# Kernel optimization log

Hardware: AMD Instinct MI355X
Metric: run time of the kernel (lower is better)

Reference implementation:

```python
import jax, jax.numpy as jnp
import numpy as np

B, S, D_MODEL = 4, 4096, 1024
H, KD, F = 16, 64, 256
KERNEL_SCALE = 1.0
NORM = 1.0 / np.sqrt(KD).astype(np.float32)  # 1/sqrt(key_dim)
EPS = 1e-6


def setup_inputs() -> dict:
    key = jax.random.key(0)
    ks = jax.random.split(key, 12)
    s = 0.02
    x = jax.random.normal(ks[0], (B, S, D_MODEL), dtype=jnp.float32)
    Wq = jax.random.normal(ks[1], (D_MODEL, H * KD), dtype=jnp.float32) * s
    bq = jnp.zeros((H * KD,), jnp.float32)
    Wk = jax.random.normal(ks[2], (D_MODEL, H * KD), dtype=jnp.float32) * s
    bk = jnp.zeros((H * KD,), jnp.float32)
    Wv = jax.random.normal(ks[3], (D_MODEL, H * KD), dtype=jnp.float32) * s
    bv = jnp.zeros((H * KD,), jnp.float32)
    # RFF params (non-trainable in original; orthogonal-ish random here)
    rff_W = jax.random.normal(ks[4], (KD, F), dtype=jnp.float32)
    q_, _ = jnp.linalg.qr(rff_W.T)  # (F, KD) -> orthonormal rows subset
    rff_W = q_.T[:KD, :F].astype(jnp.float32)
    rff_b = jax.random.uniform(ks[5], (F,), jnp.float32, 0.0, 2.0 * np.pi)
    Wo = jax.random.normal(ks[6], (H * KD, D_MODEL), dtype=jnp.float32) * s
    bo = jnp.zeros((D_MODEL,), jnp.float32)
    return {"x": x, "Wq": Wq, "bq": bq, "Wk": Wk, "bk": bk, "Wv": Wv,
            "bv": bv, "rff_W": rff_W, "rff_b": rff_b, "Wo": Wo, "bo": bo}


def _split_heads(t):
    # [B, S, H*KD] -> [B, H, S, KD]
    return t.reshape(B, S, H, KD).transpose(0, 2, 1, 3)


def _rff(t, rff_W, rff_b):
    # RandomFourierFeatures: cos((x*scale) @ W + b) * sqrt(2/F)
    proj = jnp.einsum('bhsd,df->bhsf', t * KERNEL_SCALE, rff_W) + rff_b
    return jnp.cos(proj) * np.sqrt(2.0 / F).astype(np.float32)


def reference(x, Wq, bq, Wk, bk, Wv, bv, rff_W, rff_b, Wo, bo):
    q = _split_heads(x @ Wq + bq)  # [B,H,S,KD]
    k = _split_heads(x @ Wk + bk)
    v = _split_heads(x @ Wv + bv)
    q_prime = _rff(q * NORM, rff_W, rff_b)  # [B,H,S,F]
    k_prime = _rff(k * NORM, rff_W, rff_b)
    # Non-causal FAVOR+ linear attention: O(L)
    kv = jnp.einsum('bhsf,bhsd->bhfd', k_prime, v)          # [B,H,F,KD]
    k_sum = jnp.sum(k_prime, axis=2)                         # [B,H,F]
    num = jnp.einsum('bhsf,bhfd->bhsd', q_prime, kv)         # [B,H,S,KD]
    den = jnp.einsum('bhsf,bhf->bhs', q_prime, k_sum)        # [B,H,S]
    out = num / (den + EPS)[..., None]
    out = out.transpose(0, 2, 1, 3).reshape(B, S, H * KD)    # merge heads
    return out @ Wo + bo
```

## Files before the change

### kernel.cpp

```cpp
#include <hip/hip_runtime.h>
#include <hip/hip_bf16.h>
#include <math.h>

#define B_SZ    4
#define S_LEN   4096
#define DMODEL  1024
#define NH      16
#define KDIM    64
#define NF      256
#define NROWS   (B_SZ * S_LEN)
#define RFF_SCALE 0.08838834764831845f
#define NORM_Q    0.125f

typedef __attribute__((ext_vector_type(8))) short s8v;
typedef __attribute__((ext_vector_type(4))) float f4v;

static __device__ __forceinline__ unsigned short f2bf(float f) {
  unsigned u = __float_as_uint(f);
  unsigned r = (u + 0x7FFFu + ((u >> 16) & 1u)) >> 16;
  return (unsigned short)r;
}

#define MFMA16(a, b, c) __builtin_amdgcn_mfma_f32_16x16x32_bf16((a), (b), (c), 0, 0, 0)

__device__ __forceinline__ void glds16(const void* g, void* l) {
  __builtin_amdgcn_global_load_lds(
      (const __attribute__((address_space(1))) void*)g,
      (__attribute__((address_space(3))) void*)l, 16, 0, 0);
}

__global__ __launch_bounds__(256) void cast_bf16_kernel(
    const float* __restrict__ src, unsigned short* __restrict__ dst, int n8)
{
  int i = blockIdx.x * 256 + threadIdx.x;
  if (i >= n8) return;
  const float* s = src + (size_t)i * 8;
  float4 a = *(const float4*)s;
  float4 b = *(const float4*)(s + 4);
  union { s8v v; unsigned short u[8]; } o;
  o.u[0]=f2bf(a.x); o.u[1]=f2bf(a.y); o.u[2]=f2bf(a.z); o.u[3]=f2bf(a.w);
  o.u[4]=f2bf(b.x); o.u[5]=f2bf(b.y); o.u[6]=f2bf(b.z); o.u[7]=f2bf(b.w);
  *(s8v*)(dst + (size_t)i * 8) = o.v;
}

__global__ __launch_bounds__(256) void transpose_cast_kernel(
    const float* __restrict__ W, unsigned short* __restrict__ WT)
{
  __shared__ float t[32][33];
  const int k0 = blockIdx.y * 32, n0 = blockIdx.x * 32;
  const int c = threadIdx.x & 31, r4 = threadIdx.x >> 5;
#pragma unroll
  for (int i = 0; i < 4; ++i) {
    int row = r4 + i * 8;
    t[row][c] = W[(size_t)(k0 + row) * 1024 + n0 + c];
  }
  __syncthreads();
#pragma unroll
  for (int i = 0; i < 4; ++i) {
    int row = r4 + i * 8;
    WT[(size_t)(n0 + row) * 1024 + k0 + c] = f2bf(t[c][row]);
  }
}

__global__ __launch_bounds__(256) void prep_rff_kernel(
    const float* __restrict__ rffW, unsigned short* __restrict__ rffWT)
{
  int i = blockIdx.x * 256 + threadIdx.x;
  int f = i >> 6, d = i & 63;
  rffWT[(size_t)f * 64 + d] = f2bf(rffW[(size_t)d * 256 + f] * NORM_Q);
}

template <int OUT_BF16, int QKV_FUSED>
__global__ __launch_bounds__(512, 2) void gemm_bt_kernel(
    const unsigned short* __restrict__ A,
    const unsigned short* __restrict__ BT0,
    const unsigned short* __restrict__ BT1,
    const unsigned short* __restrict__ BT2,
    const float* __restrict__ bias0, const float* __restrict__ bias1,
    const float* __restrict__ bias2,
    void* __restrict__ out0, void* __restrict__ out1, void* __restrict__ out2,
    int M, int N, int K, int NXT)
{
  __shared__ __align__(16) unsigned short As[2][16384];
  __shared__ __align__(16) unsigned short Bs[2][16384];
  const int tid = threadIdx.x;
  const int lane = tid & 63, wave = tid >> 6;

  int wg = blockIdx.x;
  {
    const int nwg = gridDim.x;
    const int q = nwg >> 3, r = nwg & 7;
    const int xcd = wg & 7, pos = wg >> 3;
    wg = (xcd < r ? xcd * (q + 1) : r * (q + 1) + (xcd - r) * q) + pos;
  }
  const int m0 = (wg / NXT) * 256;
  int ngl = (wg % NXT) * 256;
  const unsigned short* BT = BT0;
  const float* bias = bias0;
  void* outp = out0;
  if (QKV_FUSED) {
    int which = ngl >> 10;
    if (which == 1) { BT = BT1; bias = bias1; outp = out1; }
    else if (which == 2) { BT = BT2; bias = bias2; outp = out2; }
    ngl &= 1023;
  }
  const int n0 = ngl;

  const int trow = tid >> 3;
  const int g8 = (((lane & 7) ^ (trow & 7)) * 8);
  const unsigned short* aPtr = A  + (size_t)(m0 + trow) * K + g8;
  const unsigned short* bPtr = BT + (size_t)(n0 + trow) * K + g8;
  const int NT = K >> 6;

  auto STAGE = [&](int ts, int h) {
    if (ts >= NT) return;
    const int buf = ts & 1, half = h >> 1;
    const size_t go = (size_t)half * 128 * K + (size_t)ts * 64;
    if ((h & 1) == 0) {
      unsigned short* lp = &As[buf][half * 8192 + wave * 512];
      glds16(aPtr + go, lp);
      glds16(aPtr + go + (size_t)64 * K, lp + 4096);
    } else {
      unsigned short* lp = &Bs[buf][half * 8192 + wave * 512];
      glds16(bPtr + go, lp);
      glds16(bPtr + go + (size_t)64 * K, lp + 4096);
    }
  };

  const int col = lane & 15, quad = lane >> 4;
  const int wm = (wave >> 2) * 128;
  const int wn = (wave & 3) * 64;
  const int c7 = col & 7;
  const int idxA0 = (wm + col) * 64 + ((quad ^ c7) * 8);
  const int idxA1 = (wm + col) * 64 + (((4 + quad) ^ c7) * 8);
  const int idxB0 = (wn + col) * 64 + ((quad ^ c7) * 8);
  const int idxB1 = (wn + col) * 64 + (((4 + quad) ^ c7) * 8);

  f4v acc[2][4][4];
  const f4v zz = {0.f, 0.f, 0.f, 0.f};
#pragma unroll
  for (int h = 0; h < 2; ++h)
#pragma unroll
    for (int i = 0; i < 4; ++i)
#pragma unroll
      for (int j = 0; j < 4; ++j) acc[h][i][j] = zz;

  STAGE(0, 0); STAGE(0, 1); STAGE(0, 2); STAGE(0, 3);
  asm volatile("s_waitcnt vmcnt(4)" ::: "memory");
  STAGE(1, 0); STAGE(1, 1); STAGE(1, 2);
  asm volatile("s_waitcnt vmcnt(6)" ::: "memory");
  __builtin_amdgcn_s_barrier();

  for (int t = 0; t < NT; ++t) {
    const int buf = t & 1;
    const unsigned short* pA = As[buf];
    const unsigned short* pB = Bs[buf];
    s8v a0[4][2], a1[4][2], b0[2][2], b1[2][2];

#pragma unroll
    for (int x = 0; x < 4; ++x) {
      a0[x][0] = *(const s8v*)&pA[idxA0 + x * 1024];
      a0[x][1] = *(const s8v*)&pA[idxA1 + x * 1024];
    }
#pragma unroll
    for (int u = 0; u < 2; ++u) {
      b0[u][0] = *(const s8v*)&pB[idxB0 + u * 1024];
      b0[u][1] = *(const s8v*)&pB[idxB1 + u * 1024];
    }
    STAGE(t + 1, 3);
    __builtin_amdgcn_s_barrier();
    asm volatile("s_waitcnt lgkmcnt(0)" ::: "memory");
    __builtin_amdgcn_sched_barrier(0);
    __builtin_amdgcn_s_setprio(1);
#pragma unroll
    for (int x = 0; x < 4; ++x)
#pragma unroll
      for (int u = 0; u < 2; ++u) {
        acc[0][x][u] = MFMA16(a0[x][0], b0[u][0], acc[0][x][u]);
        acc[0][x][u] = MFMA16(a0[x][1], b0[u][1], acc[0][x][u]);
      }
    __builtin_amdgcn_s_setprio(0);
    __builtin_amdgcn_sched_barrier(0);
    __builtin_amdgcn_s_barrier();

#pragma unroll
    for (int x = 0; x < 4; ++x) {
      a1[x][0] = *(const s8v*)&pA[idxA0 + 4096 + x * 1024];
      a1[x][1] = *(const s8v*)&pA[idxA1 + 4096 + x * 1024];
    }
    STAGE(t + 2, 0);
    __builtin_amdgcn_s_barrier();
    asm volatile("s_waitcnt lgkmcnt(0)" ::: "memory");
    __builtin_amdgcn_sched_barrier(0);
    __builtin_amdgcn_s_setprio(1);
#pragma unroll
    for (int x = 0; x < 4; ++x)
#pragma unroll
      for (int u = 0; u < 2; ++u) {
        acc[1][x][u] = MFMA16(a1[x][0], b0[u][0], acc[1][x][u]);
        acc[1][x][u] = MFMA16(a1[x][1], b0[u][1], acc[1][x][u]);
      }
    __builtin_amdgcn_s_setprio(0);
    __builtin_amdgcn_sched_barrier(0);
    __builtin_amdgcn_s_barrier();

#pragma unroll
    for (int u = 0; u < 2; ++u) {
      b1[u][0] = *(const s8v*)&pB[idxB0 + 2048 + u * 1024];
      b1[u][1] = *(const s8v*)&pB[idxB1 + 2048 + u * 1024];
    }
    STAGE(t + 2, 1);
    __builtin_amdgcn_s_barrier();
    asm volatile("s_waitcnt lgkmcnt(0)" ::: "memory");
    __builtin_amdgcn_sched_barrier(0);
    __builtin_amdgcn_s_setprio(1);
#pragma unroll
    for (int x = 0; x < 4; ++x)
#pragma unroll
      for (int u = 0; u < 2; ++u) {
        acc[1][x][2 + u] = MFMA16(a1[x][0], b1[u][0], acc[1][x][2 + u]);
        acc[1][x][2 + u] = MFMA16(a1[x][1], b1[u][1], acc[1][x][2 + u]);
      }
    __builtin_amdgcn_s_setprio(0);
    __builtin_amdgcn_sched_barrier(0);
    __builtin_amdgcn_s_barrier();

    STAGE(t + 2, 2);
    __builtin_amdgcn_s_barrier();
    asm volatile("s_waitcnt lgkmcnt(0)" ::: "memory");
    __builtin_amdgcn_sched_barrier(0);
    __builtin_amdgcn_s_setprio(1);
#pragma unroll
    for (int x = 0; x < 4; ++x)
#pragma unroll
      for (int u = 0; u < 2; ++u) {
        acc[0][x][2 + u] = MFMA16(a0[x][0], b1[u][0], acc[0][x][2 + u]);
        acc[0][x][2 + u] = MFMA16(a0[x][1], b1[u][1], acc[0][x][2 + u]);
      }
    __builtin_amdgcn_s_setprio(0);
    __builtin_amdgcn_sched_barrier(0);
    if (t < NT - 2) asm volatile("s_waitcnt vmcnt(6)" ::: "memory");
    else            asm volatile("s_waitcnt vmcnt(0)" ::: "memory");
    __builtin_amdgcn_s_barrier();
  }

#pragma unroll
  for (int h = 0; h < 2; ++h) {
#pragma unroll
    for (int i = 0; i < 4; ++i) {
#pragma unroll
      for (int j = 0; j < 4; ++j) {
        int n = n0 + wn + j * 16 + col;
        float bv = bias[n];
#pragma unroll
        for (int r = 0; r < 4; ++r) {
          int m = m0 + wm + h * 64 + i * 16 + quad * 4 + r;
          float v = acc[h][i][j][r] + bv;
          if (OUT_BF16)
            ((unsigned short*)outp)[(size_t)m * N + n] = f2bf(v);
          else
            ((float*)outp)[(size_t)m * N + n] = v;
        }
      }
    }
  }
}

__global__ __launch_bounds__(256) void kv_kernel(
    const unsigned short* __restrict__ kg, const unsigned short* __restrict__ vg,
    const unsigned short* __restrict__ rffWT, const float* __restrict__ rffb,
    float* __restrict__ pkv)
{
  __shared__ __align__(16) unsigned short vT[80 * 72];
  __shared__ __align__(16) unsigned short kps[256 * 72];
  const int bh = blockIdx.x, chunk = blockIdx.y;
  const int b = bh >> 4, h = bh & 15;
  const int tid = threadIdx.x;
  const int lane = tid & 63, wave = tid >> 6;
  const int col = lane & 15, quad = lane >> 4;
  const f4v zz = {0.f, 0.f, 0.f, 0.f};

  s8v wf[2][4];
  float bfv[4];
#pragma unroll
  for (int ks = 0; ks < 2; ++ks)
#pragma unroll
    for (int t = 0; t < 4; ++t)
      wf[ks][t] = *(const s8v*)(rffWT +
          (size_t)(wave * 64 + t * 16 + col) * 64 + ks * 32 + quad * 8);
#pragma unroll
  for (int j = 0; j < 4; ++j) bfv[j] = rffb[wave * 64 + j * 16 + col];

  for (int e = tid; e < 1024; e += 256) {
    int r = 64 + (e >> 6), s = e & 63;
    vT[r * 72 + s] = (r == 64) ? (unsigned short)0x3F80 : (unsigned short)0;
  }

  f4v kvacc[4][5];
#pragma unroll
  for (int i = 0; i < 4; ++i)
#pragma unroll
    for (int j = 0; j < 5; ++j) kvacc[i][j] = zz;

  for (int st = 0; st < 4; ++st) {
    const int s0 = chunk * 256 + st * 64;
    __syncthreads();
#pragma unroll
    for (int i = 0; i < 2; ++i) {
      int c = tid + i * 256;
      int s = c & 63, ch = c >> 6;
      union { s8v v; unsigned short u[8]; } vv;
      vv.v = *(const s8v*)(vg + ((size_t)(b * S_LEN + s0 + s)) * DMODEL + h * KDIM + ch * 8);
#pragma unroll
      for (int j = 0; j < 8; ++j) vT[(ch * 8 + j) * 72 + s] = vv.u[j];
    }
    f4v p[4][4];
#pragma unroll
    for (int i = 0; i < 4; ++i)
#pragma unroll
      for (int j = 0; j < 4; ++j) p[i][j] = zz;
#pragma unroll
    for (int ks = 0; ks < 2; ++ks) {
      s8v af[4];
#pragma unroll
      for (int t = 0; t < 4; ++t)
        af[t] = *(const s8v*)(kg +
            ((size_t)(b * S_LEN + s0 + t * 16 + col)) * DMODEL + h * KDIM + ks * 32 + quad * 8);
#pragma unroll
      for (int i = 0; i < 4; ++i)
#pragma unroll
        for (int j = 0; j < 4; ++j) p[i][j] = MFMA16(af[i], wf[ks][j], p[i][j]);
    }
#pragma unroll
    for (int j = 0; j < 4; ++j) {
      int f = wave * 64 + j * 16 + col;
#pragma unroll
      for (int i = 0; i < 4; ++i)
#pragma unroll
        for (int r = 0; r < 4; ++r) {
          int s = i * 16 + quad * 4 + r;
          kps[f * 72 + s] = f2bf(__cosf(p[i][j][r] + bfv[j]) * RFF_SCALE);
        }
    }
    __syncthreads();
#pragma unroll
    for (int ks = 0; ks < 2; ++ks) {
      s8v af[4], bf[5];
#pragma unroll
      for (int t = 0; t < 4; ++t)
        af[t] = *(const s8v*)&kps[(wave * 64 + t * 16 + col) * 72 + ks * 32 + quad * 8];
#pragma unroll
      for (int t = 0; t < 5; ++t)
        bf[t] = *(const s8v*)&vT[(t * 16 + col) * 72 + ks * 32 + quad * 8];
#pragma unroll
      for (int i = 0; i < 4; ++i)
#pragma unroll
        for (int j = 0; j < 5; ++j)
          kvacc[i][j] = MFMA16(af[i], bf[j], kvacc[i][j]);
    }
  }
  const size_t base = ((size_t)(chunk * 64 + bh)) * NF * 80;
#pragma unroll
  for (int i = 0; i < 4; ++i)
#pragma unroll
    for (int r = 0; r < 4; ++r) {
      int f = wave * 64 + i * 16 + quad * 4 + r;
#pragma unroll
      for (int j = 0; j < 5; ++j)
        pkv[base + (size_t)f * 80 + j * 16 + col] = kvacc[i][j][r];
    }
}

__global__ __launch_bounds__(256) void reduce_kv_kernel(
    const float* __restrict__ pkv, unsigned short* __restrict__ kvT)
{
  __shared__ unsigned short lt[80 * 256];
  const int bh = blockIdx.x;
  for (int e = threadIdx.x; e < NF * 80; e += 256) {
    float s = 0.f;
#pragma unroll
    for (int c = 0; c < 16; ++c)
      s += pkv[((size_t)(c * 64 + bh)) * NF * 80 + e];
    int f = e / 80, d = e - f * 80;
    lt[d * 256 + f] = f2bf(s);
  }
  __syncthreads();
  for (int o = threadIdx.x; o < 80 * NF; o += 256)
    kvT[(size_t)bh * 80 * NF + o] = lt[o];
}

__global__ __launch_bounds__(256) void attn_kernel(
    const unsigned short* __restrict__ qg, const unsigned short* __restrict__ kvTg,
    const unsigned short* __restrict__ rffWT, const float* __restrict__ rffb,
    unsigned short* __restrict__ att)
{
  __shared__ __align__(16) unsigned short qps[64 * 264];
  __shared__ __align__(16) unsigned short kvs[80 * 264];
  const int bh = blockIdx.x;
  const int b = bh >> 4, h = bh & 15;
  const int tid = threadIdx.x;
  const int lane = tid & 63, wave = tid >> 6;
  const int col = lane & 15, quad = lane >> 4;
  const f4v zz = {0.f, 0.f, 0.f, 0.f};

  s8v wf[2][4];
  float bfv[4];
#pragma unroll
  for (int ks = 0; ks < 2; ++ks)
#pragma unroll
    for (int t = 0; t < 4; ++t)
      wf[ks][t] = *(const s8v*)(rffWT +
          (size_t)(wave * 64 + t * 16 + col) * 64 + ks * 32 + quad * 8);
#pragma unroll
  for (int j = 0; j < 4; ++j) bfv[j] = rffb[wave * 64 + j * 16 + col];

  for (int c = tid; c < 2560; c += 256) {
    int d = c >> 5, ch = c & 31;
    *(s8v*)&kvs[d * 264 + ch * 8] =
        *(const s8v*)(kvTg + (size_t)bh * 80 * NF + d * 256 + ch * 8);
  }

  for (int it = 0; it < 4; ++it) {
    const int s0 = (blockIdx.y * 4 + it) * 64;
    f4v p[4][4];
#pragma unroll
    for (int i = 0; i < 4; ++i)
#pragma unroll
      for (int j = 0; j < 4; ++j) p[i][j] = zz;
#pragma unroll
    for (int ks = 0; ks < 2; ++ks) {
      s8v af[4];
#pragma unroll
      for (int t = 0; t < 4; ++t)
        af[t] = *(const s8v*)(qg +
            ((size_t)(b * S_LEN + s0 + t * 16 + col)) * DMODEL + h * KDIM + ks * 32 + quad * 8);
#pragma unroll
      for (int i = 0; i < 4; ++i)
#pragma unroll
        for (int j = 0; j < 4; ++j) p[i][j] = MFMA16(af[i], wf[ks][j], p[i][j]);
    }
    __syncthreads();
#pragma unroll
    for (int j = 0; j < 4; ++j) {
      int f = wave * 64 + j * 16 + col;
#pragma unroll
      for (int i = 0; i < 4; ++i)
#pragma unroll
        for (int r = 0; r < 4; ++r) {
          int s = i * 16 + quad * 4 + r;
          qps[s * 264 + f] = f2bf(__cosf(p[i][j][r] + bfv[j]) * RFF_SCALE);
        }
    }
    __syncthreads();
    f4v acc[5];
#pragma unroll
    for (int j = 0; j < 5; ++j) acc[j] = zz;
#pragma unroll
    for (int k0 = 0; k0 < 256; k0 += 32) {
      s8v af = *(const s8v*)&qps[(wave * 16 + col) * 264 + k0 + quad * 8];
      s8v bf[5];
#pragma unroll
      for (int t = 0; t < 5; ++t)
        bf[t] = *(const s8v*)&kvs[(t * 16 + col) * 264 + k0 + quad * 8];
#pragma unroll
      for (int j = 0; j < 5; ++j) acc[j] = MFMA16(af, bf[j], acc[j]);
    }
    float inv[4];
#pragma unroll
    for (int r = 0; r < 4; ++r) {
      float den = __shfl(acc[4][r], lane & 48);
      inv[r] = 1.0f / (den + 1e-6f);
    }
#pragma unroll
    for (int r = 0; r < 4; ++r) {
      int m = s0 + wave * 16 + quad * 4 + r;
      size_t obase = ((size_t)(b * S_LEN + m)) * DMODEL + h * KDIM;
#pragma unroll
      for (int j = 0; j < 4; ++j)
        att[obase + j * 16 + col] = f2bf(acc[j][r] * inv[r]);
    }
  }
}

extern "C" void kernel_launch(void* const* d_in, const int* in_sizes, int n_in,
                              void* d_out, int out_size, void* d_ws, size_t ws_size,
                              hipStream_t stream)
{
  const float* x    = (const float*)d_in[0];
  const float* Wq   = (const float*)d_in[1];
  const float* bq   = (const float*)d_in[2];
  const float* Wk   = (const float*)d_in[3];
  const float* bk   = (const float*)d_in[4];
  const float* Wv   = (const float*)d_in[5];
  const float* bv   = (const float*)d_in[6];
  const float* rffW = (const float*)d_in[7];
  const float* rffb = (const float*)d_in[8];
  const float* Wo   = (const float*)d_in[9];
  const float* bo   = (const float*)d_in[10];
  float* out = (float*)d_out;

  char* w = (char*)d_ws;
  const size_t XB = (size_t)NROWS * DMODEL * 2;
  const size_t WT = (size_t)DMODEL * DMODEL * 2;
  unsigned short* xb   = (unsigned short*)(w);
  unsigned short* WqT  = (unsigned short*)(w + XB);
  unsigned short* WkT  = (unsigned short*)(w + XB + WT);
  unsigned short* WvT  = (unsigned short*)(w + XB + 2 * WT);
  unsigned short* WoT  = (unsigned short*)(w + XB + 3 * WT);
  unsigned short* rWT  = (unsigned short*)(w + XB + 4 * WT);
  char* p = w + XB + 4 * WT + 65536;
  unsigned short* qb = (unsigned short*)(p);
  unsigned short* kb = (unsigned short*)(p + XB);
  unsigned short* vb = (unsigned short*)(p + 2 * XB);
  float* pkv         = (float*)(p + 3 * XB);
  unsigned short* kvT = (unsigned short*)(p + 3 * XB + (size_t)16 * 64 * NF * 80 * 4);
  unsigned short* att = kb;

  cast_bf16_kernel<<<NROWS * DMODEL / 8 / 256, 256, 0, stream>>>(x, xb, NROWS * DMODEL / 8);
  dim3 tg(32, 32);
  transpose_cast_kernel<<<tg, 256, 0, stream>>>(Wq, WqT);
  transpose_cast_kernel<<<tg, 256, 0, stream>>>(Wk, WkT);
  transpose_cast_kernel<<<tg, 256, 0, stream>>>(Wv, WvT);
  transpose_cast_kernel<<<tg, 256, 0, stream>>>(Wo, WoT);
  prep_rff_kernel<<<64, 256, 0, stream>>>(rffW, rWT);

  gemm_bt_kernel<1, 1><<<768, 512, 0, stream>>>(
      xb, WqT, WkT, WvT, bq, bk, bv, qb, kb, vb, NROWS, DMODEL, DMODEL, 12);

  kv_kernel<<<dim3(64, 16), 256, 0, stream>>>(kb, vb, rWT, rffb, pkv);
  reduce_kv_kernel<<<64, 256, 0, stream>>>(pkv, kvT);
  attn_kernel<<<dim3(64, 16), 256, 0, stream>>>(qb, kvT, rWT, rffb, att);

  gemm_bt_kernel<0, 0><<<256, 512, 0, stream>>>(
      att, WoT, nullptr, nullptr, bo, nullptr, nullptr, out, nullptr, nullptr,
      NROWS, DMODEL, DMODEL, 4);
}
```

Baseline: 428.9 us.

## Software-pipeline GEMM LDS reads, prefetch K/V/Q tiles, halve chunk counts

The GEMM main loop is reordered so the next tile's A/B fragments are read from LDS at the end of each iteration, and the MFMA phases are regrouped with fewer barriers. The kv and attn kernels now prefetch the next 64-row K/V/Q tile into registers while the current one is computed. They also process 512 rows per block instead of 256, so each launch has half as many blocks. The reduce kernel is split across four blocks per head and sums 8 partial chunks instead of 16, and k' stores are packed into 64-bit writes. The extra prefetch registers may lower occupancy, and fewer blocks reduce parallelism in the attention kernels.

```diff
diff --git a/kernel.cpp b/kernel.cpp
--- a/kernel.cpp
+++ b/kernel.cpp
@@ -9,6 +9,7 @@
 #define KDIM    64
 #define NF      256
 #define NROWS   (B_SZ * S_LEN)
+#define NCHUNK  8
 #define RFF_SCALE 0.08838834764831845f
 #define NORM_Q    0.125f
 
@@ -146,30 +147,47 @@
       for (int j = 0; j < 4; ++j) acc[h][i][j] = zz;
 
   STAGE(0, 0); STAGE(0, 1); STAGE(0, 2); STAGE(0, 3);
-  asm volatile("s_waitcnt vmcnt(4)" ::: "memory");
   STAGE(1, 0); STAGE(1, 1); STAGE(1, 2);
   asm volatile("s_waitcnt vmcnt(6)" ::: "memory");
   __builtin_amdgcn_s_barrier();
+
+  s8v a0[4][2], a1[4][2], b0[2][2], b1[2][2];
+  {
+    const unsigned short* pA = As[0];
+    const unsigned short* pB = Bs[0];
+#pragma unroll
+    for (int u = 0; u < 2; ++u) {
+      b0[u][0] = *(const s8v*)&pB[idxB0 + u * 1024];
+      b0[u][1] = *(const s8v*)&pB[idxB1 + u * 1024];
+    }
+#pragma unroll
+    for (int x = 0; x < 4; ++x) {
+      a0[x][0] = *(const s8v*)&pA[idxA0 + x * 1024];
+      a0[x][1] = *(const s8v*)&pA[idxA1 + x * 1024];
+    }
+  }
 
   for (int t = 0; t < NT; ++t) {
     const int buf = t & 1;
     const unsigned short* pA = As[buf];
     const unsigned short* pB = Bs[buf];
-    s8v a0[4][2], a1[4][2], b0[2][2], b1[2][2];
-
-#pragma unroll
-    for (int x = 0; x < 4; ++x) {
-      a0[x][0] = *(const s8v*)&pA[idxA0 + x * 1024];
-      a0[x][1] = *(const s8v*)&pA[idxA1 + x * 1024];
-    }
-#pragma unroll
-    for (int u = 0; u < 2; ++u) {
-      b0[u][0] = *(const s8v*)&pB[idxB0 + u * 1024];
-      b0[u][1] = *(const s8v*)&pB[idxB1 + u * 1024];
-    }
-    STAGE(t + 1, 3);
+    const unsigned short* qA = As[buf ^ 1];
+    const unsigned short* qB = Bs[buf ^ 1];
+
     __builtin_amdgcn_s_barrier();
     asm volatile("s_waitcnt lgkmcnt(0)" ::: "memory");
+    __builtin_amdgcn_sched_barrier(0);
+#pragma unroll
+    for (int u = 0; u < 2; ++u) {
+      b1[u][0] = *(const s8v*)&pB[idxB0 + 2048 + u * 1024];
+      b1[u][1] = *(const s8v*)&pB[idxB1 + 2048 + u * 1024];
+    }
+    __builtin_amdgcn_sched_barrier(0);
+#pragma unroll
+    for (int x = 0; x < 4; ++x) {
+      a1[x][0] = *(const s8v*)&pA[idxA0 + 4096 + x * 1024];
+      a1[x][1] = *(const s8v*)&pA[idxA1 + 4096 + x * 1024];
+    }
     __builtin_amdgcn_sched_barrier(0);
     __builtin_amdgcn_s_setprio(1);
 #pragma unroll
@@ -181,16 +199,55 @@
       }
     __builtin_amdgcn_s_setprio(0);
     __builtin_amdgcn_sched_barrier(0);
+
     __builtin_amdgcn_s_barrier();
-
+    STAGE(t + 1, 3);
+    asm volatile("s_waitcnt lgkmcnt(8)" ::: "memory");
+    __builtin_amdgcn_sched_barrier(0);
+    __builtin_amdgcn_s_setprio(1);
+#pragma unroll
+    for (int x = 0; x < 4; ++x)
+#pragma unroll
+      for (int u = 0; u < 2; ++u) {
+        acc[0][x][2 + u] = MFMA16(a0[x][0], b1[u][0], acc[0][x][2 + u]);
+        acc[0][x][2 + u] = MFMA16(a0[x][1], b1[u][1], acc[0][x][2 + u]);
+      }
+    __builtin_amdgcn_s_setprio(0);
+    __builtin_amdgcn_sched_barrier(0);
+
+    __builtin_amdgcn_s_barrier();
+    STAGE(t + 2, 1);
+    asm volatile("s_waitcnt lgkmcnt(0)" ::: "memory");
+    __builtin_amdgcn_sched_barrier(0);
+    __builtin_amdgcn_s_setprio(1);
+#pragma unroll
+    for (int x = 0; x < 4; ++x)
+#pragma unroll
+      for (int u = 0; u < 2; ++u) {
+        acc[1][x][2 + u] = MFMA16(a1[x][0], b1[u][0], acc[1][x][2 + u]);
+        acc[1][x][2 + u] = MFMA16(a1[x][1], b1[u][1], acc[1][x][2 + u]);
+      }
+    __builtin_amdgcn_s_setprio(0);
+    __builtin_amdgcn_sched_barrier(0);
+
+    __builtin_amdgcn_s_barrier();
+    STAGE(t + 2, 0);
+    STAGE(t + 2, 2);
+    if (t < NT - 2) asm volatile("s_waitcnt vmcnt(6)" ::: "memory");
+    else            asm volatile("s_waitcnt vmcnt(0)" ::: "memory");
+    __builtin_amdgcn_sched_barrier(0);
+    s8v b0n[2][2], a0n[4][2];
+#pragma unroll
+    for (int u = 0; u < 2; ++u) {
+      b0n[u][0] = *(const s8v*)&qB[idxB0 + u * 1024];
+      b0n[u][1] = *(const s8v*)&qB[idxB1 + u * 1024];
+    }
+    __builtin_amdgcn_sched_barrier(0);
 #pragma unroll
     for (int x = 0; x < 4; ++x) {
-      a1[x][0] = *(const s8v*)&pA[idxA0 + 4096 + x * 1024];
-      a1[x][1] = *(const s8v*)&pA[idxA1 + 4096 + x * 1024];
-    }
-    STAGE(t + 2, 0);
-    __builtin_amdgcn_s_barrier();
-    asm volatile("s_waitcnt lgkmcnt(0)" ::: "memory");
+      a0n[x][0] = *(const s8v*)&qA[idxA0 + x * 1024];
+      a0n[x][1] = *(const s8v*)&qA[idxA1 + x * 1024];
+    }
     __builtin_amdgcn_sched_barrier(0);
     __builtin_amdgcn_s_setprio(1);
 #pragma unroll
@@ -202,46 +259,10 @@
       }
     __builtin_amdgcn_s_setprio(0);
     __builtin_amdgcn_sched_barrier(0);
-    __builtin_amdgcn_s_barrier();
-
-#pragma unroll
-    for (int u = 0; u < 2; ++u) {
-      b1[u][0] = *(const s8v*)&pB[idxB0 + 2048 + u * 1024];
-      b1[u][1] = *(const s8v*)&pB[idxB1 + 2048 + u * 1024];
-    }
-    STAGE(t + 2, 1);
-    __builtin_amdgcn_s_barrier();
-    asm volatile("s_waitcnt lgkmcnt(0)" ::: "memory");
-    __builtin_amdgcn_sched_barrier(0);
-    __builtin_amdgcn_s_setprio(1);
-#pragma unroll
-    for (int x = 0; x < 4; ++x)
-#pragma unroll
-      for (int u = 0; u < 2; ++u) {
-        acc[1][x][2 + u] = MFMA16(a1[x][0], b1[u][0], acc[1][x][2 + u]);
-        acc[1][x][2 + u] = MFMA16(a1[x][1], b1[u][1], acc[1][x][2 + u]);
-      }
-    __builtin_amdgcn_s_setprio(0);
-    __builtin_amdgcn_sched_barrier(0);
-    __builtin_amdgcn_s_barrier();
-
-    STAGE(t + 2, 2);
-    __builtin_amdgcn_s_barrier();
-    asm volatile("s_waitcnt lgkmcnt(0)" ::: "memory");
-    __builtin_amdgcn_sched_barrier(0);
-    __builtin_amdgcn_s_setprio(1);
-#pragma unroll
-    for (int x = 0; x < 4; ++x)
-#pragma unroll
-      for (int u = 0; u < 2; ++u) {
-        acc[0][x][2 + u] = MFMA16(a0[x][0], b1[u][0], acc[0][x][2 + u]);
-        acc[0][x][2 + u] = MFMA16(a0[x][1], b1[u][1], acc[0][x][2 + u]);
-      }
-    __builtin_amdgcn_s_setprio(0);
-    __builtin_amdgcn_sched_barrier(0);
-    if (t < NT - 2) asm volatile("s_waitcnt vmcnt(6)" ::: "memory");
-    else            asm volatile("s_waitcnt vmcnt(0)" ::: "memory");
-    __builtin_amdgcn_s_barrier();
+#pragma unroll
+    for (int u = 0; u < 2; ++u) { b0[u][0] = b0n[u][0]; b0[u][1] = b0n[u][1]; }
+#pragma unroll
+    for (int x = 0; x < 4; ++x) { a0[x][0] = a0n[x][0]; a0[x][1] = a0n[x][1]; }
   }
 
 #pragma unroll
@@ -302,45 +323,66 @@
 #pragma unroll
     for (int j = 0; j < 5; ++j) kvacc[i][j] = zz;
 
-  for (int st = 0; st < 4; ++st) {
-    const int s0 = chunk * 256 + st * 64;
+  const int sA = tid & 63,        chA = tid >> 6;
+  const int sB = (tid + 256) & 63, chB = (tid + 256) >> 6;
+
+  union U { s8v v; unsigned short u[8]; };
+  U v0, v1;
+  s8v kf[2][4];
+  {
+    const int s0 = chunk * 512;
+    v0.v = *(const s8v*)(vg + ((size_t)(b * S_LEN + s0 + sA)) * DMODEL + h * KDIM + chA * 8);
+    v1.v = *(const s8v*)(vg + ((size_t)(b * S_LEN + s0 + sB)) * DMODEL + h * KDIM + chB * 8);
+#pragma unroll
+    for (int ks = 0; ks < 2; ++ks)
+#pragma unroll
+      for (int t = 0; t < 4; ++t)
+        kf[ks][t] = *(const s8v*)(kg +
+            ((size_t)(b * S_LEN + s0 + t * 16 + col)) * DMODEL + h * KDIM + ks * 32 + quad * 8);
+  }
+
+  for (int st = 0; st < 8; ++st) {
+    const int s0 = chunk * 512 + st * 64;
     __syncthreads();
 #pragma unroll
-    for (int i = 0; i < 2; ++i) {
-      int c = tid + i * 256;
-      int s = c & 63, ch = c >> 6;
-      union { s8v v; unsigned short u[8]; } vv;
-      vv.v = *(const s8v*)(vg + ((size_t)(b * S_LEN + s0 + s)) * DMODEL + h * KDIM + ch * 8);
-#pragma unroll
-      for (int j = 0; j < 8; ++j) vT[(ch * 8 + j) * 72 + s] = vv.u[j];
-    }
+    for (int j = 0; j < 8; ++j) vT[(chA * 8 + j) * 72 + sA] = v0.u[j];
+#pragma unroll
+    for (int j = 0; j < 8; ++j) vT[(chB * 8 + j) * 72 + sB] = v1.u[j];
     f4v p[4][4];
 #pragma unroll
     for (int i = 0; i < 4; ++i)
 #pragma unroll
       for (int j = 0; j < 4; ++j) p[i][j] = zz;
 #pragma unroll
-    for (int ks = 0; ks < 2; ++ks) {
-      s8v af[4];
-#pragma unroll
-      for (int t = 0; t < 4; ++t)
-        af[t] = *(const s8v*)(kg +
-            ((size_t)(b * S_LEN + s0 + t * 16 + col)) * DMODEL + h * KDIM + ks * 32 + quad * 8);
+    for (int ks = 0; ks < 2; ++ks)
 #pragma unroll
       for (int i = 0; i < 4; ++i)
 #pragma unroll
-        for (int j = 0; j < 4; ++j) p[i][j] = MFMA16(af[i], wf[ks][j], p[i][j]);
+        for (int j = 0; j < 4; ++j) p[i][j] = MFMA16(kf[ks][i], wf[ks][j], p[i][j]);
+    U n0, n1;
+    s8v kn[2][4];
+    if (st < 7) {
+      const int s1 = s0 + 64;
+      n0.v = *(const s8v*)(vg + ((size_t)(b * S_LEN + s1 + sA)) * DMODEL + h * KDIM + chA * 8);
+      n1.v = *(const s8v*)(vg + ((size_t)(b * S_LEN + s1 + sB)) * DMODEL + h * KDIM + chB * 8);
+#pragma unroll
+      for (int ks = 0; ks < 2; ++ks)
+#pragma unroll
+        for (int t = 0; t < 4; ++t)
+          kn[ks][t] = *(const s8v*)(kg +
+              ((size_t)(b * S_LEN + s1 + t * 16 + col)) * DMODEL + h * KDIM + ks * 32 + quad * 8);
     }
 #pragma unroll
     for (int j = 0; j < 4; ++j) {
       int f = wave * 64 + j * 16 + col;
 #pragma unroll
-      for (int i = 0; i < 4; ++i)
-#pragma unroll
-        for (int r = 0; r < 4; ++r) {
-          int s = i * 16 + quad * 4 + r;
-          kps[f * 72 + s] = f2bf(__cosf(p[i][j][r] + bfv[j]) * RFF_SCALE);
-        }
+      for (int i = 0; i < 4; ++i) {
+        union { unsigned long long d; unsigned short u[4]; } pk;
+#pragma unroll
+        for (int r = 0; r < 4; ++r)
+          pk.u[r] = f2bf(__cosf(p[i][j][r] + bfv[j]) * RFF_SCALE);
+        *(unsigned long long*)&kps[f * 72 + i * 16 + quad * 4] = pk.d;
+      }
     }
     __syncthreads();
 #pragma unroll
@@ -358,6 +400,11 @@
         for (int j = 0; j < 5; ++j)
           kvacc[i][j] = MFMA16(af[i], bf[j], kvacc[i][j]);
     }
+    v0 = n0; v1 = n1;
+#pragma unroll
+    for (int ks = 0; ks < 2; ++ks)
+#pragma unroll
+      for (int t = 0; t < 4; ++t) kf[ks][t] = kn[ks][t];
   }
   const size_t base = ((size_t)(chunk * 64 + bh)) * NF * 80;
 #pragma unroll
@@ -374,19 +421,22 @@
 __global__ __launch_bounds__(256) void reduce_kv_kernel(
     const float* __restrict__ pkv, unsigned short* __restrict__ kvT)
 {
-  __shared__ unsigned short lt[80 * 256];
-  const int bh = blockIdx.x;
-  for (int e = threadIdx.x; e < NF * 80; e += 256) {
+  __shared__ unsigned short lt[80 * 64];
+  const int bh = blockIdx.x >> 2, qt = blockIdx.x & 3;
+  const int f0 = qt * 64;
+  for (int e = threadIdx.x; e < 64 * 80; e += 256) {
+    int fl = e / 80, d = e - fl * 80;
     float s = 0.f;
 #pragma unroll
-    for (int c = 0; c < 16; ++c)
-      s += pkv[((size_t)(c * 64 + bh)) * NF * 80 + e];
-    int f = e / 80, d = e - f * 80;
-    lt[d * 256 + f] = f2bf(s);
+    for (int c = 0; c < NCHUNK; ++c)
+      s += pkv[((size_t)(c * 64 + bh)) * NF * 80 + (size_t)(f0 + fl) * 80 + d];
+    lt[d * 64 + fl] = f2bf(s);
   }
   __syncthreads();
-  for (int o = threadIdx.x; o < 80 * NF; o += 256)
-    kvT[(size_t)bh * 80 * NF + o] = lt[o];
+  for (int o = threadIdx.x; o < 80 * 64; o += 256) {
+    int d = o >> 6, fl = o & 63;
+    kvT[(size_t)bh * 80 * NF + d * 256 + f0 + fl] = lt[o];
+  }
 }
 
 __global__ __launch_bounds__(256) void attn_kernel(
@@ -420,24 +470,39 @@
         *(const s8v*)(kvTg + (size_t)bh * 80 * NF + d * 256 + ch * 8);
   }
 
-  for (int it = 0; it < 4; ++it) {
-    const int s0 = (blockIdx.y * 4 + it) * 64;
+  s8v qf[2][4];
+  {
+    const int s0 = blockIdx.y * 512;
+#pragma unroll
+    for (int ks = 0; ks < 2; ++ks)
+#pragma unroll
+      for (int t = 0; t < 4; ++t)
+        qf[ks][t] = *(const s8v*)(qg +
+            ((size_t)(b * S_LEN + s0 + t * 16 + col)) * DMODEL + h * KDIM + ks * 32 + quad * 8);
+  }
+
+  for (int it = 0; it < 8; ++it) {
+    const int s0 = blockIdx.y * 512 + it * 64;
     f4v p[4][4];
 #pragma unroll
     for (int i = 0; i < 4; ++i)
 #pragma unroll
       for (int j = 0; j < 4; ++j) p[i][j] = zz;
 #pragma unroll
-    for (int ks = 0; ks < 2; ++ks) {
-      s8v af[4];
-#pragma unroll
-      for (int t = 0; t < 4; ++t)
-        af[t] = *(const s8v*)(qg +
-            ((size_t)(b * S_LEN + s0 + t * 16 + col)) * DMODEL + h * KDIM + ks * 32 + quad * 8);
+    for (int ks = 0; ks < 2; ++ks)
 #pragma unroll
       for (int i = 0; i < 4; ++i)
 #pragma unroll
-        for (int j = 0; j < 4; ++j) p[i][j] = MFMA16(af[i], wf[ks][j], p[i][j]);
+        for (int j = 0; j < 4; ++j) p[i][j] = MFMA16(qf[ks][i], wf[ks][j], p[i][j]);
+    s8v qn[2][4];
+    if (it < 7) {
+      const int s1 = s0 + 64;
+#pragma unroll
+      for (int ks = 0; ks < 2; ++ks)
+#pragma unroll
+        for (int t = 0; t < 4; ++t)
+          qn[ks][t] = *(const s8v*)(qg +
+              ((size_t)(b * S_LEN + s1 + t * 16 + col)) * DMODEL + h * KDIM + ks * 32 + quad * 8);
     }
     __syncthreads();
 #pragma unroll
@@ -479,6 +544,10 @@
       for (int j = 0; j < 4; ++j)
         att[obase + j * 16 + col] = f2bf(acc[j][r] * inv[r]);
     }
+#pragma unroll
+    for (int ks = 0; ks < 2; ++ks)
+#pragma unroll
+      for (int t = 0; t < 4; ++t) qf[ks][t] = qn[ks][t];
   }
 }
 
@@ -513,7 +582,7 @@
   unsigned short* kb = (unsigned short*)(p + XB);
   unsigned short* vb = (unsigned short*)(p + 2 * XB);
   float* pkv         = (float*)(p + 3 * XB);
-  unsigned short* kvT = (unsigned short*)(p + 3 * XB + (size_t)16 * 64 * NF * 80 * 4);
+  unsigned short* kvT = (unsigned short*)(p + 3 * XB + (size_t)NCHUNK * 64 * NF * 80 * 4);
   unsigned short* att = kb;
 
   cast_bf16_kernel<<<NROWS * DMODEL / 8 / 256, 256, 0, stream>>>(x, xb, NROWS * DMODEL / 8);
@@ -527,9 +596,9 @@
   gemm_bt_kernel<1, 1><<<768, 512, 0, stream>>>(
       xb, WqT, WkT, WvT, bq, bk, bv, qb, kb, vb, NROWS, DMODEL, DMODEL, 12);
 
-  kv_kernel<<<dim3(64, 16), 256, 0, stream>>>(kb, vb, rWT, rffb, pkv);
-  reduce_kv_kernel<<<64, 256, 0, stream>>>(pkv, kvT);
-  attn_kernel<<<dim3(64, 16), 256, 0, stream>>>(qb, kvT, rWT, rffb, att);
+  kv_kernel<<<dim3(64, NCHUNK), 256, 0, stream>>>(kb, vb, rWT, rffb, pkv);
+  reduce_kv_kernel<<<256, 256, 0, stream>>>(pkv, kvT);
+  attn_kernel<<<dim3(64, 8), 256, 0, stream>>>(qb, kvT, rWT, rffb, att);
 
   gemm_bt_kernel<0, 0><<<256, 512, 0, stream>>>(
       att, WoT, nullptr, nullptr, bo, nullptr, nullptr, out, nullptr, nullptr,
```

Result: faster. 404.1 us (-5.8%).
